# Kernel optimization log

Hardware: AMD Instinct MI355X
Metric: run time of the kernel (lower is better)

## Reference

```python
import jax, jax.numpy as jnp
import numpy as np

N = 50000          # nodes
E = 800000         # edges (before self loops)
F_IN = 16
HID = 64
HEADS = 4
C = 64             # per-head out channels (concat=False)
G = 64             # graphs in batch
NEG_SLOPE = 0.2


def setup_inputs() -> dict:
    key = jax.random.key(0)
    ks = jax.random.split(key, 20)
    inp = {
        "x": jax.random.normal(ks[0], (N, F_IN), jnp.float32),
        "edge_index": jax.random.randint(ks[1], (2, E), 0, N, jnp.int64),
        "batch": jnp.sort(jax.random.randint(ks[2], (N,), 0, G, jnp.int64)),
        "W_in": jax.random.normal(ks[3], (HID, F_IN), jnp.float32) * 0.1,
        "b_in": jnp.zeros((HID,), jnp.float32),
        "W_out": jax.random.normal(ks[4], (1, HID), jnp.float32) * 0.1,
        "b_out": jnp.zeros((1,), jnp.float32),
    }
    for l in range(3):
        inp[f"W{l}"] = jax.random.normal(ks[5 + 4 * l], (HEADS * C, HID), jnp.float32) * 0.1
        inp[f"asrc{l}"] = jax.random.normal(ks[6 + 4 * l], (HEADS, C), jnp.float32) * 0.1
        inp[f"adst{l}"] = jax.random.normal(ks[7 + 4 * l], (HEADS, C), jnp.float32) * 0.1
        inp[f"bg{l}"] = jnp.zeros((HID,), jnp.float32)
    return inp


def _gat_layer(x, W, a_src, a_dst, bias, src, dst, n):
    # x: [N, HID] -> h: [N, HEADS, C]
    h = (x @ W.T).reshape(n, HEADS, C)
    alpha_s = jnp.einsum("nhc,hc->nh", h, a_src)   # [N, H]
    alpha_d = jnp.einsum("nhc,hc->nh", h, a_dst)
    e = jax.nn.leaky_relu(alpha_s[src] + alpha_d[dst], NEG_SLOPE)  # [E', H]
    # segment softmax over incoming edges of each dst node
    m = jax.ops.segment_max(e, dst, num_segments=n)
    e = jnp.exp(e - m[dst])
    s = jax.ops.segment_sum(e, dst, num_segments=n)
    alpha = e / (s[dst] + 1e-16)                                   # [E', H]
    msg = alpha[:, :, None] * h[src]                               # [E', H, C]
    out = jax.ops.segment_sum(msg, dst, num_segments=n)            # [N, H, C]
    return out.mean(axis=1) + bias                                 # concat=False: head mean


def reference(x, W_in, b_in, W0, asrc0, adst0, bg0, W1, asrc1, adst1, bg1,
              W2, asrc2, adst2, bg2, W_out, b_out, edge_index, batch):
    n = x.shape[0]
    # add self loops (PyG GATConv default)
    loops = jnp.arange(n, dtype=edge_index.dtype)
    src = jnp.concatenate([edge_index[0], loops])
    dst = jnp.concatenate([edge_index[1], loops])

    h = x @ W_in.T + b_in
    for W, a_s, a_d, bg in ((W0, asrc0, adst0, bg0),
                            (W1, asrc1, adst1, bg1),
                            (W2, asrc2, adst2, bg2)):
        h = jax.nn.relu(_gat_layer(h, W, a_s, a_d, bg, src, dst, n))
        # dropout p=0.2 is inactive in eval mode

    # global mean pool over graphs
    sums = jax.ops.segment_sum(h, batch, num_segments=G)
    cnt = jax.ops.segment_sum(jnp.ones((n,), h.dtype), batch, num_segments=G)
    graph_emb = sums / jnp.maximum(cnt, 1.0)[:, None]              # [G, HID]

    return jax.nn.sigmoid(graph_emb @ W_out.T + b_out)             # [G, 1]
```

## Files before the change

### kernel.cpp

```cpp
#include <hip/hip_runtime.h>
#include <hip/hip_bf16.h>
#include <hip/hip_fp16.h>

#define HID 64
#define HEADS 4
#define GCNT 64
#define F_IN 16
#define NEG 0.2f
#define NBUCK 256
#define BSLOT 6144
#define SCHUNK 2048

typedef _Float16 f16x8 __attribute__((ext_vector_type(8)));
typedef float f32x4 __attribute__((ext_vector_type(4)));

__device__ __forceinline__ unsigned pack_h2(float a, float b) {
  __half2 h = __floats2half2_rn(a, b);
  union { __half2 h; unsigned u; } c;
  c.h = h;
  return c.u;
}
__device__ __forceinline__ __half2 uas_h2(unsigned u) {
  union { unsigned u; __half2 h; } c;
  c.u = u;
  return c.h;
}
__device__ __forceinline__ unsigned h2_as_u(__half2 h) {
  union { __half2 h; unsigned u; } c;
  c.h = h;
  return c.u;
}
__device__ __forceinline__ __half2 xor16_add(__half2 v) {
  unsigned u = (unsigned)__shfl_xor((int)h2_as_u(v), 16, 64);
  return __hadd2(v, uas_h2(u));
}

__global__ __launch_bounds__(256) void k_pre(
    const float* __restrict__ W0, const float* __restrict__ asrc,
    const float* __restrict__ adst, const float* __restrict__ Win,
    const float* __restrict__ bin, int* __restrict__ bcur,
    float* __restrict__ vb, float* __restrict__ c8) {
  int t = threadIdx.x;
  if (blockIdx.x == 0) {
    bcur[t] = 0;
    return;
  }
  __shared__ float vaL[512];
#pragma unroll
  for (int it = 0; it < 2; ++it) {
    int idx = t + it * 256;
    int q = idx >> 6, j = idx & 63;
    const float* a = (q < 4) ? asrc : adst;
    int h = q & 3;
    float s = 0.f;
    for (int c = 0; c < 64; ++c) s += a[h * 64 + c] * W0[(h * 64 + c) * 64 + j];
    vaL[idx] = s;
  }
  __syncthreads();
  if (t < 128) {
    int q = t >> 4, k = t & 15;
    float s = 0.f;
    for (int j = 0; j < 64; ++j) s += vaL[q * 64 + j] * Win[j * F_IN + k];
    vb[t] = s;
  } else if (t < 136) {
    int q = t - 128;
    float s = 0.f;
    for (int j = 0; j < 64; ++j) s += vaL[q * 64 + j] * bin[j];
    c8[q] = s;
  }
}

__global__ __launch_bounds__(256) void k_bucket(
    const int* __restrict__ ei, int* __restrict__ bcur,
    unsigned* __restrict__ tmp, int E, int N) {
  __shared__ int hist[NBUCK];
  __shared__ int base[NBUCK];
  int t = threadIdx.x;
  int start = blockIdx.x * SCHUNK;
  int end = min(start + SCHUNK, E + N);
  hist[t] = 0;
  __syncthreads();
  unsigned val[8];
  int rank[8];
  bool ok[8];
#pragma unroll
  for (int k = 0; k < 8; ++k) {
    int i = start + t + k * 256;
    ok[k] = i < end;
    if (ok[k]) {
      int s, d;
      if (i < E) {
        s = ei[i];
        d = ei[E + i];
      } else {
        s = d = i - E;
      }
      val[k] = ((unsigned)d << 16) | (unsigned)s;
      rank[k] = atomicAdd(&hist[d >> 8], 1);
    }
  }
  __syncthreads();
  int h = hist[t];
  base[t] = h ? atomicAdd(&bcur[t], h) : 0;
  __syncthreads();
#pragma unroll
  for (int k = 0; k < 8; ++k) {
    if (ok[k]) {
      int bk = (int)(val[k] >> 24);
      int idx = base[bk] + rank[k];
      if (idx < BSLOT) tmp[(size_t)bk * BSLOT + idx] = val[k];
    }
  }
}

__global__ __launch_bounds__(256) void k_bsort(
    const unsigned* __restrict__ tmp, const int* __restrict__ bcur,
    int* __restrict__ rowptr, int* __restrict__ col, int N) {
  __shared__ int s[NBUCK];
  __shared__ int hist[NBUCK];
  __shared__ int pref[NBUCK];
  int b = blockIdx.x, t = threadIdx.x;
  int c = min(bcur[t], BSLOT);
  s[t] = c;
  __syncthreads();
  for (int o = 1; o < 256; o <<= 1) {
    int x = (t >= o) ? s[t - o] : 0;
    __syncthreads();
    s[t] += x;
    __syncthreads();
  }
  int base = (b == 0) ? 0 : s[b - 1];
  int total = s[255];
  int cntb = min(bcur[b], BSLOT);
  hist[t] = 0;
  __syncthreads();
  for (int j = t; j < cntb; j += 256)
    atomicAdd(&hist[(tmp[(size_t)b * BSLOT + j] >> 16) & 255], 1);
  __syncthreads();
  int v = hist[t];
  pref[t] = v;
  __syncthreads();
  for (int o = 1; o < 256; o <<= 1) {
    int x = (t >= o) ? pref[t - o] : 0;
    __syncthreads();
    pref[t] += x;
    __syncthreads();
  }
  pref[t] -= v;
  __syncthreads();
  int node = b * 256 + t;
  if (node < N) rowptr[node] = base + pref[t];
  if (b == 255 && t == 255) rowptr[N] = total;
  hist[t] = 0;
  __syncthreads();
  for (int j = t; j < cntb; j += 256) {
    unsigned e = tmp[(size_t)b * BSLOT + j];
    int d8 = (int)((e >> 16) & 255);
    int r = atomicAdd(&hist[d8], 1);
    col[base + pref[d8] + r] = (int)(e & 0xffffu);
  }
}

__global__ void k_init(const float* __restrict__ x, const float* __restrict__ Win,
                       const float* __restrict__ bin,
                       const float* __restrict__ W0, const float* __restrict__ W1,
                       const float* __restrict__ W2,
                       __half* __restrict__ Wh3, __half* __restrict__ Wcat3,
                       float* __restrict__ sums, const float* __restrict__ vb,
                       const float* __restrict__ c8,
                       float* __restrict__ as_, float* __restrict__ ad_,
                       __half* __restrict__ hh, int N) {
  int b = blockIdx.x, t = threadIdx.x;
  if (b < 384) {
    int i = b * 256 + t;
    if (i < 49152) {
      const float* W = (i < 16384) ? W0 : (i < 32768) ? W1 : W2;
      Wh3[i] = __float2half(W[i & 16383]);
    } else {
      int j = i - 49152;
      int l = j >> 14;
      int r = j & 16383;
      int c = r >> 8;
      int k256 = r & 255;
      int h = k256 & 3, kk = k256 >> 2;
      const float* W = (l == 0) ? W0 : (l == 1) ? W1 : W2;
      Wcat3[j] = __float2half(0.25f * W[(h * 64 + c) * 64 + kk]);
    }
    return;
  }
  if (b < 401) {
    int i = (b - 384) * 256 + t;
    if (i < GCNT * HID + GCNT) sums[i] = 0.f;
    return;
  }
  int i = (b - 401) * 256 + t;
  if (i >= N * HID) return;
  int n = i >> 6, j = i & 63;
  const float* xr = x + (size_t)n * F_IN;
  const float* wr = Win + j * F_IN;
  float xv[F_IN];
  float acc = bin[j];
#pragma unroll
  for (int k = 0; k < F_IN; ++k) {
    xv[k] = xr[k];
    acc = fmaf(xv[k], wr[k], acc);
  }
  hh[i] = __float2half(acc);
  if (j < 8) {
    const float* vbq = vb + j * 16;
    float s = c8[j];
#pragma unroll
    for (int k = 0; k < F_IN; ++k) s = fmaf(xv[k], vbq[k], s);
    if (j < 4) as_[(size_t)n * 4 + j] = s;
    else ad_[(size_t)n * 4 + (j - 4)] = s;
  }
}

__device__ __forceinline__ void gat_one_node(
    int node, int lane, const __half* __restrict__ h, const float* __restrict__ as_,
    const float* __restrict__ ad_, const int* __restrict__ rowptr,
    const int* __restrict__ col, __half* __restrict__ Mrow) {
  int r0 = rowptr[node];
  int deg = rowptr[node + 1] - r0;
  float4 adv = *(const float4*)(ad_ + (size_t)node * 4);

  if (deg <= 64) {
    int off = 0;
    float x0 = 0.f, x1 = 0.f, x2 = 0.f, x3 = 0.f;
    if (lane < deg) {
      int s = col[r0 + lane];
      off = s << 6;
      float4 av = *(const float4*)(as_ + (size_t)s * 4);
      float e0 = av.x + adv.x; e0 = (e0 > 0.f) ? e0 : NEG * e0;
      float e1 = av.y + adv.y; e1 = (e1 > 0.f) ? e1 : NEG * e1;
      float e2 = av.z + adv.z; e2 = (e2 > 0.f) ? e2 : NEG * e2;
      float e3 = av.w + adv.w; e3 = (e3 > 0.f) ? e3 : NEG * e3;
      x0 = __expf(fminf(e0, 60.f));
      x1 = __expf(fminf(e1, 60.f));
      x2 = __expf(fminf(e2, 60.f));
      x3 = __expf(fminf(e3, 60.f));
    }
    float s0 = x0, s1 = x1, s2 = x2, s3 = x3;
#pragma unroll
    for (int o = 32; o; o >>= 1) {
      s0 += __shfl_xor(s0, o, 64);
      s1 += __shfl_xor(s1, o, 64);
      s2 += __shfl_xor(s2, o, 64);
      s3 += __shfl_xor(s3, o, 64);
    }
    unsigned w01 = pack_h2(x0 / (s0 + 1e-16f), x1 / (s1 + 1e-16f));
    unsigned w23 = pack_h2(x2 / (s2 + 1e-16f), x3 / (s3 + 1e-16f));
    __half2 acc01 = __floats2half2_rn(0.f, 0.f);
    __half2 acc23 = acc01;
#pragma unroll 4
    for (int j = 0; j < deg; ++j) {
      int oj = __builtin_amdgcn_readlane(off, j) + lane;
      unsigned W01 = __builtin_amdgcn_readlane(w01, j);
      unsigned W23 = __builtin_amdgcn_readlane(w23, j);
      __half2 hv = __half2half2(h[oj]);
      acc01 = __hfma2(hv, uas_h2(W01), acc01);
      acc23 = __hfma2(hv, uas_h2(W23), acc23);
    }
    *(__half2*)&Mrow[lane * 4] = acc01;
    *(__half2*)&Mrow[lane * 4 + 2] = acc23;
    return;
  }
  float m0 = -1e30f, m1 = -1e30f, m2 = -1e30f, m3 = -1e30f;
  for (int j = lane; j < deg; j += 64) {
    int s = col[r0 + j];
    float4 av = *(const float4*)(as_ + (size_t)s * 4);
    float e0 = av.x + adv.x; e0 = (e0 > 0.f) ? e0 : NEG * e0; m0 = fmaxf(m0, e0);
    float e1 = av.y + adv.y; e1 = (e1 > 0.f) ? e1 : NEG * e1; m1 = fmaxf(m1, e1);
    float e2 = av.z + adv.z; e2 = (e2 > 0.f) ? e2 : NEG * e2; m2 = fmaxf(m2, e2);
    float e3 = av.w + adv.w; e3 = (e3 > 0.f) ? e3 : NEG * e3; m3 = fmaxf(m3, e3);
  }
#pragma unroll
  for (int o = 32; o; o >>= 1) {
    m0 = fmaxf(m0, __shfl_xor(m0, o, 64));
    m1 = fmaxf(m1, __shfl_xor(m1, o, 64));
    m2 = fmaxf(m2, __shfl_xor(m2, o, 64));
    m3 = fmaxf(m3, __shfl_xor(m3, o, 64));
  }
  float s0 = 0.f, s1 = 0.f, s2 = 0.f, s3 = 0.f;
  for (int j = lane; j < deg; j += 64) {
    int s = col[r0 + j];
    float4 av = *(const float4*)(as_ + (size_t)s * 4);
    float e0 = av.x + adv.x; e0 = (e0 > 0.f) ? e0 : NEG * e0; s0 += __expf(e0 - m0);
    float e1 = av.y + adv.y; e1 = (e1 > 0.f) ? e1 : NEG * e1; s1 += __expf(e1 - m1);
    float e2 = av.z + adv.z; e2 = (e2 > 0.f) ? e2 : NEG * e2; s2 += __expf(e2 - m2);
    float e3 = av.w + adv.w; e3 = (e3 > 0.f) ? e3 : NEG * e3; s3 += __expf(e3 - m3);
  }
#pragma unroll
  for (int o = 32; o; o >>= 1) {
    s0 += __shfl_xor(s0, o, 64);
    s1 += __shfl_xor(s1, o, 64);
    s2 += __shfl_xor(s2, o, 64);
    s3 += __shfl_xor(s3, o, 64);
  }
  float i0 = 1.f / (s0 + 1e-16f), i1 = 1.f / (s1 + 1e-16f);
  float i2 = 1.f / (s2 + 1e-16f), i3 = 1.f / (s3 + 1e-16f);
  float a0 = 0.f, a1 = 0.f, a2 = 0.f, a3 = 0.f;
  for (int j = 0; j < deg; ++j) {
    int s = col[r0 + j];
    float4 av = *(const float4*)(as_ + (size_t)s * 4);
    float e0 = av.x + adv.x; e0 = (e0 > 0.f) ? e0 : NEG * e0;
    float e1 = av.y + adv.y; e1 = (e1 > 0.f) ? e1 : NEG * e1;
    float e2 = av.z + adv.z; e2 = (e2 > 0.f) ? e2 : NEG * e2;
    float e3 = av.w + adv.w; e3 = (e3 > 0.f) ? e3 : NEG * e3;
    float hv = __half2float(h[(s << 6) + lane]);
    a0 = fmaf(__expf(e0 - m0) * i0, hv, a0);
    a1 = fmaf(__expf(e1 - m1) * i1, hv, a1);
    a2 = fmaf(__expf(e2 - m2) * i2, hv, a2);
    a3 = fmaf(__expf(e3 - m3) * i3, hv, a3);
  }
  *(__half2*)&Mrow[lane * 4] = __floats2half2_rn(a0, a1);
  *(__half2*)&Mrow[lane * 4 + 2] = __floats2half2_rn(a2, a3);
}

__device__ __forceinline__ void gat_pair(
    int pr, int lane, int half, int l5, int N,
    const __half* __restrict__ h, const float* __restrict__ as_,
    const float* __restrict__ ad_, const int* __restrict__ rowptr,
    const int* __restrict__ col, __half* __restrict__ Mt) {
  int n0 = pr * 2;
  int n1 = min(n0 + 1, N - 1);
  int mynode = half ? n1 : n0;
  int r0 = rowptr[mynode];
  int dg = rowptr[mynode + 1] - r0;
  int dgA = __builtin_amdgcn_readlane(dg, 0);
  int dgB = __builtin_amdgcn_readlane(dg, 32);

  if (dgA <= 32 && dgB <= 32) {
    float4 adv = *(const float4*)(ad_ + (size_t)mynode * 4);
    int off = 0;
    float x0 = 0.f, x1 = 0.f, x2 = 0.f, x3 = 0.f;
    if (l5 < dg) {
      int s = col[r0 + l5];
      off = s << 6;
      float4 av = *(const float4*)(as_ + (size_t)s * 4);
      float e0 = av.x + adv.x; e0 = (e0 > 0.f) ? e0 : NEG * e0;
      float e1 = av.y + adv.y; e1 = (e1 > 0.f) ? e1 : NEG * e1;
      float e2 = av.z + adv.z; e2 = (e2 > 0.f) ? e2 : NEG * e2;
      float e3 = av.w + adv.w; e3 = (e3 > 0.f) ? e3 : NEG * e3;
      x0 = __expf(fminf(e0, 60.f));
      x1 = __expf(fminf(e1, 60.f));
      x2 = __expf(fminf(e2, 60.f));
      x3 = __expf(fminf(e3, 60.f));
    }
    float s0 = x0, s1 = x1, s2 = x2, s3 = x3;
#pragma unroll
    for (int o = 16; o; o >>= 1) {
      s0 += __shfl_xor(s0, o, 64);
      s1 += __shfl_xor(s1, o, 64);
      s2 += __shfl_xor(s2, o, 64);
      s3 += __shfl_xor(s3, o, 64);
    }
    unsigned w01 = pack_h2(x0 / (s0 + 1e-16f), x1 / (s1 + 1e-16f));
    unsigned w23 = pack_h2(x2 / (s2 + 1e-16f), x3 / (s3 + 1e-16f));

    int g = l5 >> 4, li = l5 & 15;
    const uint2* h4p = (const uint2*)h;
    __half2 z = __floats2half2_rn(0.f, 0.f);
    __half2 a0_01 = z, a0_23 = z, a1_01 = z, a1_23 = z;
    __half2 a2_01 = z, a2_23 = z, a3_01 = z, a3_23 = z;
    int mdeg = max(dgA, dgB);
    int baddr = half << 7;
#pragma unroll 2
    for (int j = 0; j < mdeg; j += 2) {
      int addr = baddr + (j + g) * 4;
      int oj = __builtin_amdgcn_ds_bpermute(addr, off);
      unsigned W01 = (unsigned)__builtin_amdgcn_ds_bpermute(addr, (int)w01);
      unsigned W23 = (unsigned)__builtin_amdgcn_ds_bpermute(addr, (int)w23);
      uint2 hv = h4p[(oj >> 2) + li];
      __half2 ha = uas_h2(hv.x), hb = uas_h2(hv.y);
      __half2 wA = uas_h2(W01), wB = uas_h2(W23);
      __half2 c0 = __low2half2(ha), c1 = __high2half2(ha);
      __half2 c2 = __low2half2(hb), c3 = __high2half2(hb);
      a0_01 = __hfma2(c0, wA, a0_01); a0_23 = __hfma2(c0, wB, a0_23);
      a1_01 = __hfma2(c1, wA, a1_01); a1_23 = __hfma2(c1, wB, a1_23);
      a2_01 = __hfma2(c2, wA, a2_01); a2_23 = __hfma2(c2, wB, a2_23);
      a3_01 = __hfma2(c3, wA, a3_01); a3_23 = __hfma2(c3, wB, a3_23);
    }
    a0_01 = xor16_add(a0_01); a0_23 = xor16_add(a0_23);
    a1_01 = xor16_add(a1_01); a1_23 = xor16_add(a1_23);
    a2_01 = xor16_add(a2_01); a2_23 = xor16_add(a2_23);
    a3_01 = xor16_add(a3_01); a3_23 = xor16_add(a3_23);
    if (g == 0) {
      __half* row = &Mt[(mynode & 15) * 264 + li * 16];
      uint4 st1, st2;
      st1.x = h2_as_u(a0_01); st1.y = h2_as_u(a0_23);
      st1.z = h2_as_u(a1_01); st1.w = h2_as_u(a1_23);
      st2.x = h2_as_u(a2_01); st2.y = h2_as_u(a2_23);
      st2.z = h2_as_u(a3_01); st2.w = h2_as_u(a3_23);
      *(uint4*)&row[0] = st1;
      *(uint4*)&row[8] = st2;
    }
  } else {
    gat_one_node(n0, lane, h, as_, ad_, rowptr, col, &Mt[(n0 & 15) * 264]);
    if (n1 != n0) gat_one_node(n1, lane, h, as_, ad_, rowptr, col, &Mt[(n1 & 15) * 264]);
  }
}

template <bool FIN>
__global__ __launch_bounds__(256) void k_gatf(
    const __half* __restrict__ h, const float* __restrict__ as_,
    const float* __restrict__ ad_, const int* __restrict__ rowptr,
    const int* __restrict__ col, const __half* __restrict__ Wcat,
    const float* __restrict__ bg, const __half* __restrict__ Wn,
    const float* __restrict__ asrc, const float* __restrict__ adst,
    __half* __restrict__ hout, float* __restrict__ nas, float* __restrict__ nad,
    int N) {
  __shared__ __half Mt[16 * 264];
  __shared__ __half O[16 * 72];
  int tid = threadIdx.x;
  int lane = tid & 63, wv = tid >> 6;
  int tile = blockIdx.x;
  int half = lane >> 5, l5 = lane & 31;
  int npairs = (N + 1) >> 1;

  int pr0 = tile * 8 + wv * 2;
  int pr1 = pr0 + 1;
  bool has0 = pr0 < npairs, has1 = pr1 < npairs;
  if (has0 && has1) {
    int my0 = min(pr0 * 2 + half, N - 1);
    int my1 = min(pr1 * 2 + half, N - 1);
    int r0a = rowptr[my0];
    int dga = rowptr[my0 + 1] - r0a;
    int r0b = rowptr[my1];
    int dgb = rowptr[my1 + 1] - r0b;
    int dA0 = __builtin_amdgcn_readlane(dga, 0);
    int dB0 = __builtin_amdgcn_readlane(dga, 32);
    int dA1 = __builtin_amdgcn_readlane(dgb, 0);
    int dB1 = __builtin_amdgcn_readlane(dgb, 32);

    if (dA0 <= 32 && dB0 <= 32 && dA1 <= 32 && dB1 <= 32) {
      float4 adva = *(const float4*)(ad_ + (size_t)my0 * 4);
      float4 advb = *(const float4*)(ad_ + (size_t)my1 * 4);
      int offa = 0, offb = 0;
      float xa0 = 0.f, xa1 = 0.f, xa2 = 0.f, xa3 = 0.f;
      float xb0 = 0.f, xb1 = 0.f, xb2 = 0.f, xb3 = 0.f;
      if (l5 < dga) {
        int s = col[r0a + l5];
        offa = s << 6;
        float4 av = *(const float4*)(as_ + (size_t)s * 4);
        float e0 = av.x + adva.x; e0 = (e0 > 0.f) ? e0 : NEG * e0;
        float e1 = av.y + adva.y; e1 = (e1 > 0.f) ? e1 : NEG * e1;
        float e2 = av.z + adva.z; e2 = (e2 > 0.f) ? e2 : NEG * e2;
        float e3 = av.w + adva.w; e3 = (e3 > 0.f) ? e3 : NEG * e3;
        xa0 = __expf(fminf(e0, 60.f));
        xa1 = __expf(fminf(e1, 60.f));
        xa2 = __expf(fminf(e2, 60.f));
        xa3 = __expf(fminf(e3, 60.f));
      }
      if (l5 < dgb) {
        int s = col[r0b + l5];
        offb = s << 6;
        float4 av = *(const float4*)(as_ + (size_t)s * 4);
        float e0 = av.x + advb.x; e0 = (e0 > 0.f) ? e0 : NEG * e0;
        float e1 = av.y + advb.y; e1 = (e1 > 0.f) ? e1 : NEG * e1;
        float e2 = av.z + advb.z; e2 = (e2 > 0.f) ? e2 : NEG * e2;
        float e3 = av.w + advb.w; e3 = (e3 > 0.f) ? e3 : NEG * e3;
        xb0 = __expf(fminf(e0, 60.f));
        xb1 = __expf(fminf(e1, 60.f));
        xb2 = __expf(fminf(e2, 60.f));
        xb3 = __expf(fminf(e3, 60.f));
      }
      float sa0 = xa0, sa1 = xa1, sa2 = xa2, sa3 = xa3;
      float sb0 = xb0, sb1 = xb1, sb2 = xb2, sb3 = xb3;
#pragma unroll
      for (int o = 16; o; o >>= 1) {
        sa0 += __shfl_xor(sa0, o, 64);
        sa1 += __shfl_xor(sa1, o, 64);
        sa2 += __shfl_xor(sa2, o, 64);
        sa3 += __shfl_xor(sa3, o, 64);
        sb0 += __shfl_xor(sb0, o, 64);
        sb1 += __shfl_xor(sb1, o, 64);
        sb2 += __shfl_xor(sb2, o, 64);
        sb3 += __shfl_xor(sb3, o, 64);
      }
      unsigned w01a = pack_h2(xa0 / (sa0 + 1e-16f), xa1 / (sa1 + 1e-16f));
      unsigned w23a = pack_h2(xa2 / (sa2 + 1e-16f), xa3 / (sa3 + 1e-16f));
      unsigned w01b = pack_h2(xb0 / (sb0 + 1e-16f), xb1 / (sb1 + 1e-16f));
      unsigned w23b = pack_h2(xb2 / (sb2 + 1e-16f), xb3 / (sb3 + 1e-16f));

      uint4* EB = (uint4*)&Mt[wv * 1056];
      EB[half * 32 + l5] = make_uint4((unsigned)offa, w01a, w23a, 0u);
      EB[64 + half * 32 + l5] = make_uint4((unsigned)offb, w01b, w23b, 0u);

      int g = l5 >> 4, li = l5 & 15;
      const uint2* h4p = (const uint2*)h;
      __half2 z = __floats2half2_rn(0.f, 0.f);
      __half2 pa0 = z, pa1 = z, pa2 = z, pa3 = z, pa4 = z, pa5 = z, pa6 = z, pa7 = z;
      __half2 pb0 = z, pb1 = z, pb2 = z, pb3 = z, pb4 = z, pb5 = z, pb6 = z, pb7 = z;
      int mm = max(max(dA0, dB0), max(dA1, dB1));
      int ebase = half * 32;
#pragma unroll 2
      for (int j = 0; j < mm; j += 2) {
        uint4 ra = EB[ebase + j + g];
        uint4 rb = EB[64 + ebase + j + g];
        uint2 hva = h4p[((int)ra.x >> 2) + li];
        uint2 hvb = h4p[((int)rb.x >> 2) + li];
        {
          __half2 ha = uas_h2(hva.x), hb = uas_h2(hva.y);
          __half2 wA = uas_h2(ra.y), wB = uas_h2(ra.z);
          __half2 c0 = __low2half2(ha), c1 = __high2half2(ha);
          __half2 c2 = __low2half2(hb), c3 = __high2half2(hb);
          pa0 = __hfma2(c0, wA, pa0); pa1 = __hfma2(c0, wB, pa1);
          pa2 = __hfma2(c1, wA, pa2); pa3 = __hfma2(c1, wB, pa3);
          pa4 = __hfma2(c2, wA, pa4); pa5 = __hfma2(c2, wB, pa5);
          pa6 = __hfma2(c3, wA, pa6); pa7 = __hfma2(c3, wB, pa7);
        }
        {
          __half2 ha = uas_h2(hvb.x), hb = uas_h2(hvb.y);
          __half2 wA = uas_h2(rb.y), wB = uas_h2(rb.z);
          __half2 c0 = __low2half2(ha), c1 = __high2half2(ha);
          __half2 c2 = __low2half2(hb), c3 = __high2half2(hb);
          pb0 = __hfma2(c0, wA, pb0); pb1 = __hfma2(c0, wB, pb1);
          pb2 = __hfma2(c1, wA, pb2); pb3 = __hfma2(c1, wB, pb3);
          pb4 = __hfma2(c2, wA, pb4); pb5 = __hfma2(c2, wB, pb5);
          pb6 = __hfma2(c3, wA, pb6); pb7 = __hfma2(c3, wB, pb7);
        }
      }
      pa0 = xor16_add(pa0); pa1 = xor16_add(pa1); pa2 = xor16_add(pa2); pa3 = xor16_add(pa3);
      pa4 = xor16_add(pa4); pa5 = xor16_add(pa5); pa6 = xor16_add(pa6); pa7 = xor16_add(pa7);
      pb0 = xor16_add(pb0); pb1 = xor16_add(pb1); pb2 = xor16_add(pb2); pb3 = xor16_add(pb3);
      pb4 = xor16_add(pb4); pb5 = xor16_add(pb5); pb6 = xor16_add(pb6); pb7 = xor16_add(pb7);
      if (g == 0) {
        __half* rowA = &Mt[(my0 & 15) * 264 + li * 16];
        __half* rowB = &Mt[(my1 & 15) * 264 + li * 16];
        uint4 s1, s2;
        s1.x = h2_as_u(pa0); s1.y = h2_as_u(pa1); s1.z = h2_as_u(pa2); s1.w = h2_as_u(pa3);
        s2.x = h2_as_u(pa4); s2.y = h2_as_u(pa5); s2.z = h2_as_u(pa6); s2.w = h2_as_u(pa7);
        *(uint4*)&rowA[0] = s1;
        *(uint4*)&rowA[8] = s2;
        s1.x = h2_as_u(pb0); s1.y = h2_as_u(pb1); s1.z = h2_as_u(pb2); s1.w = h2_as_u(pb3);
        s2.x = h2_as_u(pb4); s2.y = h2_as_u(pb5); s2.z = h2_as_u(pb6); s2.w = h2_as_u(pb7);
        *(uint4*)&rowB[0] = s1;
        *(uint4*)&rowB[8] = s2;
      }
    } else {
      gat_pair(pr0, lane, half, l5, N, h, as_, ad_, rowptr, col, Mt);
      gat_pair(pr1, lane, half, l5, N, h, as_, ad_, rowptr, col, Mt);
    }
  } else if (has0) {
    gat_pair(pr0, lane, half, l5, N, h, as_, ad_, rowptr, col, Mt);
  }
  __syncthreads();

  int quad = lane >> 4, n16 = lane & 15;
  const f16x8* WC = (const f16x8*)Wcat;
  int ch1 = wv * 16 + n16;
  float bias1 = bg[ch1];
  f32x4 c1 = {0.f, 0.f, 0.f, 0.f};
#pragma unroll
  for (int i = 0; i < 8; ++i) {
    f16x8 a = *(const f16x8*)&Mt[n16 * 264 + (i * 4 + quad) * 8];
    c1 = __builtin_amdgcn_mfma_f32_16x16x32_f16(a, WC[ch1 * 32 + i * 4 + quad], c1, 0, 0, 0);
  }
#pragma unroll
  for (int r = 0; r < 4; ++r) {
    float v = fmaxf(c1[r] + bias1, 0.f);
    O[(quad * 4 + r) * 72 + ch1] = __float2half(v);
  }
  __syncthreads();
  {
    int nd = tid >> 4, c0 = (tid & 15) * 4;
    int node = tile * 16 + nd;
    if (node < N) {
      uint2 v = *(const uint2*)&O[nd * 72 + c0];
      *(uint2*)&hout[(size_t)node * 64 + c0] = v;
    }
  }
  if (!FIN) {
    const f16x8* WN = (const f16x8*)Wn;
    f16x8 a0 = *(const f16x8*)&O[n16 * 72 + quad * 8];
    f16x8 a1 = *(const f16x8*)&O[n16 * 72 + 32 + quad * 8];
    f32x4 accs[4];
#pragma unroll
    for (int nt = 0; nt < 4; ++nt) {
      int ch = wv * 64 + nt * 16 + n16;
      f32x4 zz = {0.f, 0.f, 0.f, 0.f};
      zz = __builtin_amdgcn_mfma_f32_16x16x32_f16(a0, WN[ch * 8 + quad], zz, 0, 0, 0);
      zz = __builtin_amdgcn_mfma_f32_16x16x32_f16(a1, WN[ch * 8 + 4 + quad], zz, 0, 0, 0);
      accs[nt] = zz;
    }
#pragma unroll
    for (int r = 0; r < 4; ++r) {
      float vs = 0.f, vd = 0.f;
#pragma unroll
      for (int nt = 0; nt < 4; ++nt) {
        int ch = wv * 64 + nt * 16 + n16;
        vs = fmaf(accs[nt][r], asrc[ch], vs);
        vd = fmaf(accs[nt][r], adst[ch], vd);
      }
#pragma unroll
      for (int o = 8; o; o >>= 1) {
        vs += __shfl_xor(vs, o, 64);
        vd += __shfl_xor(vd, o, 64);
      }
      int node = tile * 16 + quad * 4 + r;
      if (n16 == 0 && node < N) {
        nas[(size_t)node * 4 + wv] = vs;
        nad[(size_t)node * 4 + wv] = vd;
      }
    }
  }
}

__global__ __launch_bounds__(256) void k_pool(
    const __half* __restrict__ hh, const int* __restrict__ batch,
    float* __restrict__ sums, float* __restrict__ cnt, int N) {
  int c = threadIdx.x & 63, r = threadIdx.x >> 6;
  int base = blockIdx.x * 64 + r * 16;
  float acc = 0.f;
  int curg = -1, cacc = 0;
  for (int i = 0; i < 16; ++i) {
    int n = base + i;
    if (n >= N) break;
    int g = batch[n];
    if (g != curg) {
      if (curg >= 0) {
        atomicAdd(&sums[curg * HID + c], acc);
        if (c == 0) atomicAdd(&cnt[curg], (float)cacc);
      }
      curg = g; acc = 0.f; cacc = 0;
    }
    acc += __half2float(hh[(size_t)n * HID + c]);
    cacc++;
  }
  if (curg >= 0) {
    atomicAdd(&sums[curg * HID + c], acc);
    if (c == 0) atomicAdd(&cnt[curg], (float)cacc);
  }
}

__global__ void k_out(const float* __restrict__ sums, const float* __restrict__ cnt,
                      const float* __restrict__ Wout, const float* __restrict__ bout,
                      float* __restrict__ out) {
  int g = blockIdx.x, lane = threadIdx.x;
  float cg = fmaxf(cnt[g], 1.f);
  float v = (sums[g * HID + lane] / cg) * Wout[lane];
#pragma unroll
  for (int o = 32; o; o >>= 1) v += __shfl_xor(v, o, 64);
  if (lane == 0) out[g] = 1.f / (1.f + __expf(-v));
}

extern "C" void kernel_launch(void* const* d_in, const int* in_sizes, int n_in,
                              void* d_out, int out_size, void* d_ws, size_t ws_size,
                              hipStream_t stream) {
  const float* x    = (const float*)d_in[0];
  const int*   ei   = (const int*)d_in[1];
  const int*   batch= (const int*)d_in[2];
  const float* Win  = (const float*)d_in[3];
  const float* bin  = (const float*)d_in[4];
  const float* Wout = (const float*)d_in[5];
  const float* bout = (const float*)d_in[6];
  const float* Wl[3]    = {(const float*)d_in[7],  (const float*)d_in[11], (const float*)d_in[15]};
  const float* asrcl[3] = {(const float*)d_in[8],  (const float*)d_in[12], (const float*)d_in[16]};
  const float* adstl[3] = {(const float*)d_in[9],  (const float*)d_in[13], (const float*)d_in[17]};
  const float* bgl[3]   = {(const float*)d_in[10], (const float*)d_in[14], (const float*)d_in[18]};

  int N = in_sizes[2];
  int E = in_sizes[1] / 2;
  int EE = E + N;

  char* p = (char*)d_ws;
  auto alloc = [&](size_t bytes) {
    char* r = p;
    p += (bytes + 255) & ~(size_t)255;
    return r;
  };
  int*      rowptr = (int*)alloc((size_t)(N + 1) * 4);
  int*      col    = (int*)alloc((size_t)EE * 4);
  unsigned* tmp    = (unsigned*)alloc((size_t)NBUCK * BSLOT * 4);
  int*      bcur   = (int*)alloc(NBUCK * 4);
  float*    vb     = (float*)alloc(128 * 4);
  float*    c8     = (float*)alloc(8 * 4);
  __half*   hhA    = (__half*)alloc((size_t)N * HID * 2);
  __half*   hhB    = (__half*)alloc((size_t)N * HID * 2);
  float*    asA    = (float*)alloc((size_t)N * HEADS * 4);
  float*    adA    = (float*)alloc((size_t)N * HEADS * 4);
  float*    asB    = (float*)alloc((size_t)N * HEADS * 4);
  float*    adB    = (float*)alloc((size_t)N * HEADS * 4);
  __half*   Wh3    = (__half*)alloc(3 * 16384 * 2);
  __half*   Wcat3  = (__half*)alloc(3 * 16384 * 2);
  float*    sums   = (float*)alloc((size_t)(GCNT * HID + GCNT) * 4);
  float*    cnt    = sums + GCNT * HID;

  int tiles = (N + 15) / 16;

  k_pre<<<2, 256, 0, stream>>>(Wl[0], asrcl[0], adstl[0], Win, bin, bcur, vb, c8);
  k_bucket<<<(EE + SCHUNK - 1) / SCHUNK, 256, 0, stream>>>(ei, bcur, tmp, E, N);
  k_bsort<<<NBUCK, 256, 0, stream>>>(tmp, bcur, rowptr, col, N);

  k_init<<<401 + (N * HID + 255) / 256, 256, 0, stream>>>(
      x, Win, bin, Wl[0], Wl[1], Wl[2], Wh3, Wcat3, sums, vb, c8, asA, adA, hhA, N);

  k_gatf<false><<<tiles, 256, 0, stream>>>(hhA, asA, adA, rowptr, col,
                                           Wcat3, bgl[0], Wh3 + 16384, asrcl[1], adstl[1],
                                           hhB, asB, adB, N);
  k_gatf<false><<<tiles, 256, 0, stream>>>(hhB, asB, adB, rowptr, col,
                                           Wcat3 + 16384, bgl[1], Wh3 + 32768, asrcl[2], adstl[2],
                                           hhA, asA, adA, N);
  k_gatf<true><<<tiles, 256, 0, stream>>>(hhA, asA, adA, rowptr, col,
                                          Wcat3 + 32768, bgl[2], nullptr, nullptr, nullptr,
                                          hhB, nullptr, nullptr, N);

  k_pool<<<(N + 63) / 64, 256, 0, stream>>>(hhB, batch, sums, cnt, N);
  k_out<<<GCNT, 64, 0, stream>>>(sums, cnt, Wout, bout, (float*)d_out);
}
```

Before: 334.5 us.

## Fuse global mean pooling into final GAT layer and unroll edge gather

The last GAT layer now adds its ReLU outputs straight into per-graph sums and counts with atomics, taken from the MFMA accumulators. This removes the separate pooling kernel and the final half-precision feature write and read-back. The neighbour aggregation loop is unrolled to process eight edges per iteration with the trip count padded to a multiple of eight, so more gathers are in flight at once. A launch-bounds occupancy hint is also added. The padding relies on the unused edge-buffer slots carrying zero weight, and the extra live registers could limit occupancy.

```diff
diff --git a/kernel.cpp b/kernel.cpp
--- a/kernel.cpp
+++ b/kernel.cpp
@@ -34,6 +34,18 @@
   unsigned u = (unsigned)__shfl_xor((int)h2_as_u(v), 16, 64);
   return __hadd2(v, uas_h2(u));
 }
+
+#define FMA_REC(HV, W01, W23, P0, P1, P2, P3, P4, P5, P6, P7)      \
+  do {                                                             \
+    __half2 _ha = uas_h2((HV).x), _hb = uas_h2((HV).y);            \
+    __half2 _wA = uas_h2(W01), _wB = uas_h2(W23);                  \
+    __half2 _c0 = __low2half2(_ha), _c1 = __high2half2(_ha);       \
+    __half2 _c2 = __low2half2(_hb), _c3 = __high2half2(_hb);       \
+    P0 = __hfma2(_c0, _wA, P0); P1 = __hfma2(_c0, _wB, P1);        \
+    P2 = __hfma2(_c1, _wA, P2); P3 = __hfma2(_c1, _wB, P3);        \
+    P4 = __hfma2(_c2, _wA, P4); P5 = __hfma2(_c2, _wB, P5);        \
+    P6 = __hfma2(_c3, _wA, P6); P7 = __hfma2(_c3, _wB, P7);        \
+  } while (0)
 
 __global__ __launch_bounds__(256) void k_pre(
     const float* __restrict__ W0, const float* __restrict__ asrc,
@@ -402,13 +414,14 @@
 }
 
 template <bool FIN>
-__global__ __launch_bounds__(256) void k_gatf(
+__global__ __launch_bounds__(256, 4) void k_gatf(
     const __half* __restrict__ h, const float* __restrict__ as_,
     const float* __restrict__ ad_, const int* __restrict__ rowptr,
     const int* __restrict__ col, const __half* __restrict__ Wcat,
     const float* __restrict__ bg, const __half* __restrict__ Wn,
     const float* __restrict__ asrc, const float* __restrict__ adst,
     __half* __restrict__ hout, float* __restrict__ nas, float* __restrict__ nad,
+    const int* __restrict__ batchv, float* __restrict__ gsums,
     int N) {
   __shared__ __half Mt[16 * 264];
   __shared__ __half O[16 * 72];
@@ -493,33 +506,31 @@
       __half2 pa0 = z, pa1 = z, pa2 = z, pa3 = z, pa4 = z, pa5 = z, pa6 = z, pa7 = z;
       __half2 pb0 = z, pb1 = z, pb2 = z, pb3 = z, pb4 = z, pb5 = z, pb6 = z, pb7 = z;
       int mm = max(max(dA0, dB0), max(dA1, dB1));
-      int ebase = half * 32;
+      int mmr = (mm + 7) & ~7;
+      int eA = half * 32 + g;
+      int eB = 64 + half * 32 + g;
 #pragma unroll 2
-      for (int j = 0; j < mm; j += 2) {
-        uint4 ra = EB[ebase + j + g];
-        uint4 rb = EB[64 + ebase + j + g];
-        uint2 hva = h4p[((int)ra.x >> 2) + li];
-        uint2 hvb = h4p[((int)rb.x >> 2) + li];
-        {
-          __half2 ha = uas_h2(hva.x), hb = uas_h2(hva.y);
-          __half2 wA = uas_h2(ra.y), wB = uas_h2(ra.z);
-          __half2 c0 = __low2half2(ha), c1 = __high2half2(ha);
-          __half2 c2 = __low2half2(hb), c3 = __high2half2(hb);
-          pa0 = __hfma2(c0, wA, pa0); pa1 = __hfma2(c0, wB, pa1);
-          pa2 = __hfma2(c1, wA, pa2); pa3 = __hfma2(c1, wB, pa3);
-          pa4 = __hfma2(c2, wA, pa4); pa5 = __hfma2(c2, wB, pa5);
-          pa6 = __hfma2(c3, wA, pa6); pa7 = __hfma2(c3, wB, pa7);
-        }
-        {
-          __half2 ha = uas_h2(hvb.x), hb = uas_h2(hvb.y);
-          __half2 wA = uas_h2(rb.y), wB = uas_h2(rb.z);
-          __half2 c0 = __low2half2(ha), c1 = __high2half2(ha);
-          __half2 c2 = __low2half2(hb), c3 = __high2half2(hb);
-          pb0 = __hfma2(c0, wA, pb0); pb1 = __hfma2(c0, wB, pb1);
-          pb2 = __hfma2(c1, wA, pb2); pb3 = __hfma2(c1, wB, pb3);
-          pb4 = __hfma2(c2, wA, pb4); pb5 = __hfma2(c2, wB, pb5);
-          pb6 = __hfma2(c3, wA, pb6); pb7 = __hfma2(c3, wB, pb7);
-        }
+      for (int j = 0; j < mmr; j += 8) {
+        uint4 a0 = EB[eA + j],     a1 = EB[eA + j + 2];
+        uint4 a2 = EB[eA + j + 4], a3 = EB[eA + j + 6];
+        uint4 b0 = EB[eB + j],     b1 = EB[eB + j + 2];
+        uint4 b2 = EB[eB + j + 4], b3 = EB[eB + j + 6];
+        uint2 vA0 = h4p[((int)a0.x >> 2) + li];
+        uint2 vA1 = h4p[((int)a1.x >> 2) + li];
+        uint2 vA2 = h4p[((int)a2.x >> 2) + li];
+        uint2 vA3 = h4p[((int)a3.x >> 2) + li];
+        uint2 vB0 = h4p[((int)b0.x >> 2) + li];
+        uint2 vB1 = h4p[((int)b1.x >> 2) + li];
+        uint2 vB2 = h4p[((int)b2.x >> 2) + li];
+        uint2 vB3 = h4p[((int)b3.x >> 2) + li];
+        FMA_REC(vA0, a0.y, a0.z, pa0, pa1, pa2, pa3, pa4, pa5, pa6, pa7);
+        FMA_REC(vA1, a1.y, a1.z, pa0, pa1, pa2, pa3, pa4, pa5, pa6, pa7);
+        FMA_REC(vA2, a2.y, a2.z, pa0, pa1, pa2, pa3, pa4, pa5, pa6, pa7);
+        FMA_REC(vA3, a3.y, a3.z, pa0, pa1, pa2, pa3, pa4, pa5, pa6, pa7);
+        FMA_REC(vB0, b0.y, b0.z, pb0, pb1, pb2, pb3, pb4, pb5, pb6, pb7);
+        FMA_REC(vB1, b1.y, b1.z, pb0, pb1, pb2, pb3, pb4, pb5, pb6, pb7);
+        FMA_REC(vB2, b2.y, b2.z, pb0, pb1, pb2, pb3, pb4, pb5, pb6, pb7);
+        FMA_REC(vB3, b3.y, b3.z, pb0, pb1, pb2, pb3, pb4, pb5, pb6, pb7);
       }
       pa0 = xor16_add(pa0); pa1 = xor16_add(pa1); pa2 = xor16_add(pa2); pa3 = xor16_add(pa3);
       pa4 = xor16_add(pa4); pa5 = xor16_add(pa5); pa6 = xor16_add(pa6); pa7 = xor16_add(pa7);
@@ -557,6 +568,38 @@
     f16x8 a = *(const f16x8*)&Mt[n16 * 264 + (i * 4 + quad) * 8];
     c1 = __builtin_amdgcn_mfma_f32_16x16x32_f16(a, WC[ch1 * 32 + i * 4 + quad], c1, 0, 0, 0);
   }
+
+  if (FIN) {
+    float* cnt_ = gsums + GCNT * HID;
+    int curg = -1;
+    float acc = 0.f;
+    int cacc = 0;
+#pragma unroll
+    for (int r = 0; r < 4; ++r) {
+      int node = tile * 16 + quad * 4 + r;
+      if (node < N) {
+        int gph = batchv[node];
+        float v = fmaxf(c1[r] + bias1, 0.f);
+        if (gph != curg) {
+          if (curg >= 0) {
+            atomicAdd(&gsums[curg * HID + ch1], acc);
+            if (ch1 == 0) atomicAdd(&cnt_[curg], (float)cacc);
+          }
+          curg = gph;
+          acc = 0.f;
+          cacc = 0;
+        }
+        acc += v;
+        ++cacc;
+      }
+    }
+    if (curg >= 0) {
+      atomicAdd(&gsums[curg * HID + ch1], acc);
+      if (ch1 == 0) atomicAdd(&cnt_[curg], (float)cacc);
+    }
+    return;
+  }
+
 #pragma unroll
   for (int r = 0; r < 4; ++r) {
     float v = fmaxf(c1[r] + bias1, 0.f);
@@ -571,7 +614,7 @@
       *(uint2*)&hout[(size_t)node * 64 + c0] = v;
     }
   }
-  if (!FIN) {
+  {
     const f16x8* WN = (const f16x8*)Wn;
     f16x8 a0 = *(const f16x8*)&O[n16 * 72 + quad * 8];
     f16x8 a1 = *(const f16x8*)&O[n16 * 72 + 32 + quad * 8];
@@ -604,33 +647,6 @@
         nad[(size_t)node * 4 + wv] = vd;
       }
     }
-  }
-}
-
-__global__ __launch_bounds__(256) void k_pool(
-    const __half* __restrict__ hh, const int* __restrict__ batch,
-    float* __restrict__ sums, float* __restrict__ cnt, int N) {
-  int c = threadIdx.x & 63, r = threadIdx.x >> 6;
-  int base = blockIdx.x * 64 + r * 16;
-  float acc = 0.f;
-  int curg = -1, cacc = 0;
-  for (int i = 0; i < 16; ++i) {
-    int n = base + i;
-    if (n >= N) break;
-    int g = batch[n];
-    if (g != curg) {
-      if (curg >= 0) {
-        atomicAdd(&sums[curg * HID + c], acc);
-        if (c == 0) atomicAdd(&cnt[curg], (float)cacc);
-      }
-      curg = g; acc = 0.f; cacc = 0;
-    }
-    acc += __half2float(hh[(size_t)n * HID + c]);
-    cacc++;
-  }
-  if (curg >= 0) {
-    atomicAdd(&sums[curg * HID + c], acc);
-    if (c == 0) atomicAdd(&cnt[curg], (float)cacc);
   }
 }
 
@@ -698,14 +714,15 @@
 
   k_gatf<false><<<tiles, 256, 0, stream>>>(hhA, asA, adA, rowptr, col,
                                            Wcat3, bgl[0], Wh3 + 16384, asrcl[1], adstl[1],
-                                           hhB, asB, adB, N);
+                                           hhB, asB, adB, nullptr, nullptr, N);
   k_gatf<false><<<tiles, 256, 0, stream>>>(hhB, asB, adB, rowptr, col,
                                            Wcat3 + 16384, bgl[1], Wh3 + 32768, asrcl[2], adstl[2],
-                                           hhA, asA, adA, N);
+                                           hhA, asA, adA, nullptr, nullptr, N);
   k_gatf<true><<<tiles, 256, 0, stream>>>(hhA, asA, adA, rowptr, col,
                                           Wcat3 + 32768, bgl[2], nullptr, nullptr, nullptr,
-                                          hhB, nullptr, nullptr, N);
-
-  k_pool<<<(N + 63) / 64, 256, 0, stream>>>(hhB, batch, sums, cnt, N);
+                                          nullptr, nullptr, nullptr, batch, sums, N);
+
+  k_pool_removed:;
+
   k_out<<<GCNT, 64, 0, stream>>>(sums, cnt, Wout, bout, (float*)d_out);
 }
```

Result: slower. 394.5 us (+17.9%).
